# Kernel tuning notes

Measured on AMD Instinct MI355X. Metric: run time of the kernel, lower is better.

## Reference

```python
import jax, jax.numpy as jnp
import numpy as np

GROUP_SIZE = 128  # per-group quantization granularity along infeatures (K)


def setup_inputs() -> dict:
    key = jax.random.key(0)
    k1, k2, k3, k4, k5 = jax.random.split(key, 5)
    B, K, N, G = 32, 4096, 11008, 4096 // GROUP_SIZE
    x = jax.random.normal(k1, (B, K), dtype=jnp.float16)
    # packed int4 weights: 8 nibbles per int32 along K
    qweight = jax.random.randint(k2, (K // 8, N), 0, 2**31 - 1, dtype=jnp.int32)
    # packed int4 zero points: 8 nibbles per int32 along N, one row per group
    qzeros = jax.random.randint(k3, (G, N // 8), 0, 2**31 - 1, dtype=jnp.int32)
    scales = (jax.random.uniform(k4, (G, N), dtype=jnp.float16) * 0.02 + 0.001).astype(jnp.float16)
    bias = (jax.random.normal(k5, (N,), dtype=jnp.float16) * 0.01).astype(jnp.float16)
    return {"x": x, "qweight": qweight, "qzeros": qzeros, "scales": scales, "bias": bias}


def _unpack_int4(packed, axis):
    # packed int32 -> 8 unsigned 4-bit values, expanded along `axis`
    shifts = (jnp.arange(8, dtype=jnp.int32) * 4)
    shape = [1] * (packed.ndim + 1)
    shape[axis + 1] = 8
    vals = (jnp.expand_dims(packed, axis + 1) >> shifts.reshape(shape)) & 0xF
    new_shape = list(packed.shape)
    new_shape[axis] *= 8
    return vals.reshape(new_shape)


def reference(x, qweight, qzeros, scales, bias):
    K = qweight.shape[0] * 8
    N = qweight.shape[1]
    G = scales.shape[0]
    # unpack weights along K: [K, N] int32 in [0, 15]
    q = _unpack_int4(qweight, axis=0)
    # unpack zero points along N: [G, N]
    z = _unpack_int4(qzeros, axis=1)
    # GPTQ dequant: W[k, n] = scales[g(k), n] * (q[k, n] - (z[g(k), n] + 1))
    qg = q.reshape(G, GROUP_SIZE, N)
    W = ((qg - (z + 1)[:, None, :]).astype(jnp.float16) * scales[:, None, :]).reshape(K, N)
    out = jnp.matmul(x, W, preferred_element_type=jnp.float32).astype(jnp.float16)
    return out + bias
```

## Files before the change

### kernel.cpp

```cpp
#include <hip/hip_runtime.h>
#include <hip/hip_bf16.h>


#define M_ROWS 32
#define K_DIM  4096
#define N_DIM  11008
#define GS     128
#define BN     32
#define KSPLIT 8
#define BKR    (K_DIM / KSPLIT)
#define NGRP   (BKR / GS)
#define LDSW   33

typedef _Float16 f16x2 __attribute__((ext_vector_type(2)));
typedef _Float16 f16x8 __attribute__((ext_vector_type(8)));
typedef unsigned int u32x4 __attribute__((ext_vector_type(4)));
typedef float  f32x4  __attribute__((ext_vector_type(4)));

__global__ __launch_bounds__(256)
void pack_x_kernel(const float* __restrict__ x, _Float16* __restrict__ xp) {
    const int gt = blockIdx.x * 256 + threadIdx.x;
    const int c  = gt >> 6;
    const int l  = gt & 63;
    const int t  = c & 1;
    const int b  = c >> 1;
    const int m  = 16 * t + (l & 15);
    const int k0 = 32 * b + (l >> 4) * 8;
    const float4 f0 = *(const float4*)(&x[m * K_DIM + k0]);
    const float4 f1 = *(const float4*)(&x[m * K_DIM + k0 + 4]);
    f16x8 hv;
    hv[0] = (_Float16)f0.x; hv[1] = (_Float16)f1.x;
    hv[2] = (_Float16)f0.y; hv[3] = (_Float16)f1.y;
    hv[4] = (_Float16)f0.z; hv[5] = (_Float16)f1.z;
    hv[6] = (_Float16)f0.w; hv[7] = (_Float16)f1.w;
    *(f16x8*)(&xp[(size_t)gt * 8]) = hv;
}

__device__ inline f16x8 dequant_word(unsigned w, f16x2 scv, f16x2 zv) {
    const f16x2 k1024 = {(_Float16)1024, (_Float16)1024};
    u32x4 u;
    #pragma unroll
    for (int i = 0; i < 4; ++i) {
        const unsigned t = ((w >> (4 * i)) & 0x000F000Fu) | 0x64006400u;
        f16x2 p = __builtin_bit_cast(f16x2, t);
        p = p - k1024;
        p = __builtin_elementwise_fma(p, scv, zv);
        u[i] = __builtin_bit_cast(unsigned, p);
    }
    return __builtin_bit_cast(f16x8, u);
}

__global__ __launch_bounds__(512, 4)
void gptq_fused_kernel(const _Float16* __restrict__ xp,
                       const int* __restrict__ qweight,
                       const int* __restrict__ qzeros,
                       const float* __restrict__ scales,
                       const float* __restrict__ bias,
                       float* __restrict__ out)
{
    __shared__ float lds[KSPLIT * M_ROWS * LDSW];

    const int tid  = threadIdx.x;
    const int lane = tid & 63;
    const int kb   = tid >> 6;
    const int n0   = blockIdx.x * BN;

    const int col  = lane & 15;
    const int quad = lane >> 4;
    const int nA   = n0 + col;
    const int nB   = n0 + 16 + col;

    f32x4 accA0 = {0.f,0.f,0.f,0.f}, accA1 = {0.f,0.f,0.f,0.f};
    f32x4 accB0 = {0.f,0.f,0.f,0.f}, accB1 = {0.f,0.f,0.f,0.f};

    #pragma unroll
    for (int gl = 0; gl < NGRP; ++gl) {
        const int g   = kb * NGRP + gl;
        const int zwA = qzeros[g * (N_DIM / 8) + (nA >> 3)];
        const int zwB = qzeros[g * (N_DIM / 8) + (nB >> 3)];
        const float scA = scales[g * N_DIM + nA];
        const float scB = scales[g * N_DIM + nB];
        const float zsA = -((float)(((zwA >> ((nA & 7) * 4)) & 0xF) + 1)) * scA;
        const float zsB = -((float)(((zwB >> ((nB & 7) * 4)) & 0xF) + 1)) * scB;
        const f16x2 scvA = {(_Float16)scA, (_Float16)scA};
        const f16x2 scvB = {(_Float16)scB, (_Float16)scB};
        const f16x2 zvA  = {(_Float16)zsA, (_Float16)zsA};
        const f16x2 zvB  = {(_Float16)zsB, (_Float16)zsB};

        #pragma unroll
        for (int ks = 0; ks < 4; ++ks) {
            const int wrow = kb * (BKR / 8) + gl * (GS / 8) + ks * 4 + quad;
            const unsigned wA = (unsigned)qweight[wrow * N_DIM + nA];
            const unsigned wB = (unsigned)qweight[wrow * N_DIM + nB];
            const f16x8 bfA = dequant_word(wA, scvA, zvA);
            const f16x8 bfB = dequant_word(wB, scvB, zvB);
            const int b = kb * 16 + gl * 4 + ks;
            const f16x8 a0 = *(const f16x8*)(&xp[((b * 2 + 0) * 64 + lane) * 8]);
            const f16x8 a1 = *(const f16x8*)(&xp[((b * 2 + 1) * 64 + lane) * 8]);
            accA0 = __builtin_amdgcn_mfma_f32_16x16x32_f16(a0, bfA, accA0, 0, 0, 0);
            accA1 = __builtin_amdgcn_mfma_f32_16x16x32_f16(a1, bfA, accA1, 0, 0, 0);
            accB0 = __builtin_amdgcn_mfma_f32_16x16x32_f16(a0, bfB, accB0, 0, 0, 0);
            accB1 = __builtin_amdgcn_mfma_f32_16x16x32_f16(a1, bfB, accB1, 0, 0, 0);
        }
    }

    float* slab = &lds[kb * M_ROWS * LDSW];
    #pragma unroll
    for (int r = 0; r < 4; ++r) {
        const int m = quad * 4 + r;
        slab[m * LDSW + col]             = accA0[r];
        slab[(16 + m) * LDSW + col]      = accA1[r];
        slab[m * LDSW + 16 + col]        = accB0[r];
        slab[(16 + m) * LDSW + 16 + col] = accB1[r];
    }
    __syncthreads();

    #pragma unroll
    for (int i = 0; i < 2; ++i) {
        const int idx = i * 512 + tid;
        const int m   = idx >> 5;
        const int c   = idx & 31;
        float s = 0.f;
        #pragma unroll
        for (int w = 0; w < KSPLIT; ++w)
            s += lds[w * M_ROWS * LDSW + m * LDSW + c];
        out[m * N_DIM + n0 + c] = s + bias[n0 + c];
    }
}

extern "C" void kernel_launch(void* const* d_in, const int* in_sizes, int n_in,
                              void* d_out, int out_size, void* d_ws, size_t ws_size,
                              hipStream_t stream) {
    const float* x       = (const float*)d_in[0];
    const int*   qweight = (const int*)d_in[1];
    const int*   qzeros  = (const int*)d_in[2];
    const float* scales  = (const float*)d_in[3];
    const float* bias    = (const float*)d_in[4];
    float*       out     = (float*)d_out;

    _Float16* xp = (_Float16*)d_ws;

    pack_x_kernel<<<64, 256, 0, stream>>>(x, xp);
    gptq_fused_kernel<<<N_DIM / BN, 512, 0, stream>>>(xp, qweight, qzeros,
                                                      scales, bias, out);
}
```

Baseline: 84.15 us.

## Split K across two blocks per column tile with atomic accumulation

Doubles the grid by splitting K into two halves handled by separate blocks, each reducing its 8 warp slices in LDS and then atomically adding into the output. The bias is pre-written into the output by the pack kernel, so the atomics accumulate on top of it. This is meant to raise occupancy and memory-level parallelism on the weight stream, since 344 blocks underfill the GPU. The cost is float atomics on the output, an extra output initialization pass, and a nondeterministic summation order.

```diff
diff --git a/kernel.cpp b/kernel.cpp
--- a/kernel.cpp
+++ b/kernel.cpp
@@ -1,5 +1,4 @@
 #include <hip/hip_runtime.h>
-#include <hip/hip_bf16.h>
 
 
 #define M_ROWS 32
@@ -8,7 +7,8 @@
 #define GS     128
 #define BN     32
 #define KSPLIT 8
-#define BKR    (K_DIM / KSPLIT)
+#define KHALF  2
+#define BKR    (K_DIM / (KSPLIT * KHALF))
 #define NGRP   (BKR / GS)
 #define LDSW   33
 
@@ -17,23 +17,35 @@
 typedef unsigned int u32x4 __attribute__((ext_vector_type(4)));
 typedef float  f32x4  __attribute__((ext_vector_type(4)));
 
-__global__ __launch_bounds__(256)
-void pack_x_kernel(const float* __restrict__ x, _Float16* __restrict__ xp) {
-    const int gt = blockIdx.x * 256 + threadIdx.x;
-    const int c  = gt >> 6;
-    const int l  = gt & 63;
-    const int t  = c & 1;
-    const int b  = c >> 1;
-    const int m  = 16 * t + (l & 15);
-    const int k0 = 32 * b + (l >> 4) * 8;
-    const float4 f0 = *(const float4*)(&x[m * K_DIM + k0]);
-    const float4 f1 = *(const float4*)(&x[m * K_DIM + k0 + 4]);
-    f16x8 hv;
-    hv[0] = (_Float16)f0.x; hv[1] = (_Float16)f1.x;
-    hv[2] = (_Float16)f0.y; hv[3] = (_Float16)f1.y;
-    hv[4] = (_Float16)f0.z; hv[5] = (_Float16)f1.z;
-    hv[6] = (_Float16)f0.w; hv[7] = (_Float16)f1.w;
-    *(f16x8*)(&xp[(size_t)gt * 8]) = hv;
+__global__ __launch_bounds__(128)
+void pack_init_kernel(const float* __restrict__ x, const float* __restrict__ bias,
+                      _Float16* __restrict__ xp, float* __restrict__ out) {
+    const int gt = blockIdx.x * 128 + threadIdx.x;
+    if (gt < 16384) {
+        const int c  = gt >> 6;
+        const int l  = gt & 63;
+        const int t  = c & 1;
+        const int b  = c >> 1;
+        const int m  = 16 * t + (l & 15);
+        const int k0 = 32 * b + (l >> 4) * 8;
+        const float4 f0 = *(const float4*)(&x[m * K_DIM + k0]);
+        const float4 f1 = *(const float4*)(&x[m * K_DIM + k0 + 4]);
+        f16x8 hv;
+        hv[0] = (_Float16)f0.x; hv[1] = (_Float16)f1.x;
+        hv[2] = (_Float16)f0.y; hv[3] = (_Float16)f1.y;
+        hv[4] = (_Float16)f0.z; hv[5] = (_Float16)f1.z;
+        hv[6] = (_Float16)f0.w; hv[7] = (_Float16)f1.w;
+        *(f16x8*)(&xp[(size_t)gt * 8]) = hv;
+    }
+    const float4* b4 = (const float4*)bias;
+    float4*       o4 = (float4*)out;
+    #pragma unroll
+    for (int i = 0; i < 3; ++i) {
+        const int idx = gt + i * 32768;
+        if (idx < (M_ROWS * N_DIM / 4)) {
+            o4[idx] = b4[idx % (N_DIM / 4)];
+        }
+    }
 }
 
 __device__ inline f16x8 dequant_word(unsigned w, f16x2 scv, f16x2 zv) {
@@ -55,7 +67,6 @@
                        const int* __restrict__ qweight,
                        const int* __restrict__ qzeros,
                        const float* __restrict__ scales,
-                       const float* __restrict__ bias,
                        float* __restrict__ out)
 {
     __shared__ float lds[KSPLIT * M_ROWS * LDSW];
@@ -63,7 +74,9 @@
     const int tid  = threadIdx.x;
     const int lane = tid & 63;
     const int kb   = tid >> 6;
-    const int n0   = blockIdx.x * BN;
+    const int kh   = blockIdx.x & 1;
+    const int n0   = (blockIdx.x >> 1) * BN;
+    const int slice = kh * KSPLIT + kb;
 
     const int col  = lane & 15;
     const int quad = lane >> 4;
@@ -75,7 +88,7 @@
 
     #pragma unroll
     for (int gl = 0; gl < NGRP; ++gl) {
-        const int g   = kb * NGRP + gl;
+        const int g   = slice * NGRP + gl;
         const int zwA = qzeros[g * (N_DIM / 8) + (nA >> 3)];
         const int zwB = qzeros[g * (N_DIM / 8) + (nB >> 3)];
         const float scA = scales[g * N_DIM + nA];
@@ -89,12 +102,12 @@
 
         #pragma unroll
         for (int ks = 0; ks < 4; ++ks) {
-            const int wrow = kb * (BKR / 8) + gl * (GS / 8) + ks * 4 + quad;
+            const int wrow = slice * (BKR / 8) + gl * (GS / 8) + ks * 4 + quad;
             const unsigned wA = (unsigned)qweight[wrow * N_DIM + nA];
             const unsigned wB = (unsigned)qweight[wrow * N_DIM + nB];
             const f16x8 bfA = dequant_word(wA, scvA, zvA);
             const f16x8 bfB = dequant_word(wB, scvB, zvB);
-            const int b = kb * 16 + gl * 4 + ks;
+            const int b = slice * 8 + gl * 4 + ks;
             const f16x8 a0 = *(const f16x8*)(&xp[((b * 2 + 0) * 64 + lane) * 8]);
             const f16x8 a1 = *(const f16x8*)(&xp[((b * 2 + 1) * 64 + lane) * 8]);
             accA0 = __builtin_amdgcn_mfma_f32_16x16x32_f16(a0, bfA, accA0, 0, 0, 0);
@@ -119,12 +132,12 @@
     for (int i = 0; i < 2; ++i) {
         const int idx = i * 512 + tid;
         const int m   = idx >> 5;
-        const int c   = idx & 31;
-        float s = 0.f;
+        const int cc  = idx & 31;
+        float sum = 0.f;
         #pragma unroll
         for (int w = 0; w < KSPLIT; ++w)
-            s += lds[w * M_ROWS * LDSW + m * LDSW + c];
-        out[m * N_DIM + n0 + c] = s + bias[n0 + c];
+            sum += lds[w * M_ROWS * LDSW + m * LDSW + cc];
+        atomicAdd(&out[m * N_DIM + n0 + cc], sum);
     }
 }
 
@@ -140,7 +153,7 @@
 
     _Float16* xp = (_Float16*)d_ws;
 
-    pack_x_kernel<<<64, 256, 0, stream>>>(x, xp);
-    gptq_fused_kernel<<<N_DIM / BN, 512, 0, stream>>>(xp, qweight, qzeros,
-                                                      scales, bias, out);
+    pack_init_kernel<<<256, 128, 0, stream>>>(x, bias, xp, out);
+    gptq_fused_kernel<<<(N_DIM / BN) * KHALF, 512, 0, stream>>>(xp, qweight, qzeros,
+                                                                scales, out);
 }
```

Result: no change. 84.15 us (+0.0%).
